# Performance work log

Measured on AMD Instinct MI355X. Metric: run time of the kernel, lower is better.

The kernel has to match this reference:

```python
import jax, jax.numpy as jnp
import numpy as np

VOCAB = 32000
NUM_STATE = 256
NLABEL = 64
BATCH = 128
MAXLEN = 256
# transition init scale chosen so E[e^2]*S*a^2/3 ~= 1 -> per-step magnitude ~constant
TRANS_A = 0.208


def setup_inputs() -> dict:
    key = jax.random.key(0)
    k1, k2, k3, k4 = jax.random.split(key, 4)
    sentences = jax.random.randint(k1, (BATCH, MAXLEN), 0, VOCAB, dtype=jnp.int64)
    # original init: input.weight ~ U(0.5, 0.5) (constant 0.5). Use U(0.25, 0.75) so the
    # emission stays bounded away from 0 (it is divided by) while not being degenerate.
    emb = jax.random.uniform(k2, (VOCAB, NUM_STATE), minval=0.25, maxval=0.75, dtype=jnp.float32)
    transition = jax.random.uniform(k3, (NUM_STATE, NUM_STATE), minval=-TRANS_A, maxval=TRANS_A, dtype=jnp.float32)
    output = jax.random.uniform(k4, (NUM_STATE, NLABEL), minval=-0.5, maxval=0.5, dtype=jnp.float32)
    return {"sentences": sentences, "emb": emb, "transition": transition, "output": output}


def reference(sentences, emb, transition, output):
    # emission: [maxlen, batch, num_state]
    em = emb[sentences.T]

    def step_fwd(carry, e):  # carry: [B,S]
        nxt = jnp.einsum('ij,bj->bi', transition, carry) * e
        return nxt, nxt

    _, fw_rest = jax.lax.scan(step_fwd, em[0], em[1:])
    forwards = jnp.concatenate([em[:1], fw_rest], axis=0)  # [L,B,S]

    em_rev = em[::-1]

    def step_bwd(carry, e):  # uses transition^T
        nxt = jnp.einsum('ji,bj->bi', transition, carry) * e
        return nxt, nxt

    _, bw_rest = jax.lax.scan(step_bwd, em_rev[0], em_rev[1:])
    backwards = jnp.concatenate([em_rev[:1], bw_rest], axis=0)[::-1]  # time-aligned [L,B,S]

    expected_count = forwards * backwards / em
    score = jnp.einsum('lbs,sn->lbn', expected_count, output)
    return score.transpose(1, 0, 2)  # [batch, maxlen, nlabel]
```

## Files before the change

### kernel.cpp

```cpp
#include <hip/hip_runtime.h>
#include <hip/hip_bf16.h>


typedef _Float16 half8 __attribute__((ext_vector_type(8)));
typedef _Float16 half4 __attribute__((ext_vector_type(4)));
typedef __bf16 bf16x8 __attribute__((ext_vector_type(8)));
typedef __bf16 bf16x4 __attribute__((ext_vector_type(4)));
typedef float  f32x4  __attribute__((ext_vector_type(4)));
typedef unsigned long long u64;

#define LL 256
#define BB 128
#define SS 256
#define BT 16
#define RSTR8 67
#define LO_SCALE 2048.0f
#define LO_UNSCALE 4.8828125e-4f

static __device__ __forceinline__ f32x4 mfma16f(half8 a, half8 b, f32x4 c) {
  return __builtin_amdgcn_mfma_f32_16x16x32_f16(a, b, c, 0, 0, 0);
}
static __device__ __forceinline__ f32x4 mfma16(bf16x8 a, bf16x8 b, f32x4 c) {
  return __builtin_amdgcn_mfma_f32_16x16x32_bf16(a, b, c, 0, 0, 0);
}

static __device__ __forceinline__ void lds_barrier() {
  __asm__ __volatile__("s_waitcnt lgkmcnt(0)\n\ts_barrier" ::: "memory");
}

static __device__ __forceinline__ half8 read_frag_h(const u64* plane, int m, int kt, int q) {
  const int o = m * RSTR8 + kt * 8 + q * 2;
  union { u64 u[2]; half8 v; } x;
  x.u[0] = plane[o];
  x.u[1] = plane[o + 1];
  return x.v;
}
static __device__ __forceinline__ bf16x8 read_frag_b(const u64* plane, int m, int kt, int q) {
  const int o = m * RSTR8 + kt * 8 + q * 2;
  union { u64 u[2]; bf16x8 v; } x;
  x.u[0] = plane[o];
  x.u[1] = plane[o + 1];
  return x.v;
}

static __device__ __forceinline__ void write_h4f(u64* plane, int m, int c8, half4 h) {
  union { half4 v; u64 u; } x;
  x.v = h;
  plane[m * RSTR8 + c8] = x.u;
}
static __device__ __forceinline__ void write_h4b(u64* plane, int m, int c8, bf16x4 h) {
  union { bf16x4 v; u64 u; } x;
  x.v = h;
  plane[m * RSTR8 + c8] = x.u;
}

__global__ __launch_bounds__(512, 2)
void hmm_chain(const int* __restrict__ sent, const float* __restrict__ emb,
               const float* __restrict__ T, float* __restrict__ fwbuf,
               float* __restrict__ gbuf)
{
  __shared__ u64 s_carry[2][BT * RSTR8];
  __shared__ int s_tok[BT * 257];

  const int tid  = threadIdx.x;
  const int lane = tid & 63;
  const int w    = tid >> 6;
  const int m    = lane & 15;
  const int q    = lane >> 4;

  const int  bid = blockIdx.x;
  const bool fwd = (bid < 8);
  const int  bg0 = (fwd ? bid : bid - 8) * BT;
  float* const obuf = fwd ? fwbuf : gbuf;

  for (int idx = tid; idx < BT * LL; idx += 512) {
    int bb = idx >> 8, l2 = idx & 255;
    s_tok[bb * 257 + l2] = sent[(bg0 + bb) * LL + l2];
  }
  __syncthreads();

  half8 a_hi[2][8], a_lo[2][8];
#pragma unroll
  for (int mt = 0; mt < 2; ++mt) {
#pragma unroll
    for (int kt = 0; kt < 8; ++kt) {
      const int r0 = 32 * w + 16 * mt + m;
      const int kb = 32 * kt + 8 * q;
      float v[8];
      if (fwd) {
        f32x4 f0 = *(const f32x4*)(T + r0 * 256 + kb);
        f32x4 f1 = *(const f32x4*)(T + r0 * 256 + kb + 4);
#pragma unroll
        for (int j = 0; j < 4; ++j) { v[j] = f0[j]; v[4 + j] = f1[j]; }
      } else {
#pragma unroll
        for (int j = 0; j < 8; ++j) v[j] = T[(kb + j) * 256 + r0];
      }
      half8 hi, lo;
#pragma unroll
      for (int j = 0; j < 8; ++j) {
        _Float16 h = (_Float16)v[j];
        hi[j] = h;
        lo[j] = (_Float16)((v[j] - (float)h) * LO_SCALE);
      }
      a_hi[mt][kt] = hi; a_lo[mt][kt] = lo;
    }
  }

  const int l0 = fwd ? 0 : (LL - 1);
  {
    const int tok0 = s_tok[m * 257 + l0];
#pragma unroll
    for (int mt = 0; mt < 2; ++mt) {
      const int st = 32 * w + 16 * mt + 4 * q;
      f32x4 e0 = *(const f32x4*)(emb + (size_t)tok0 * 256 + st);
      f32x4 outv = e0;
      if (!fwd) outv = 1.0f;
      *(f32x4*)(obuf + ((size_t)(l0 * BB + bg0 + m)) * 256 + st) = outv;
      half4 h4;
#pragma unroll
      for (int r = 0; r < 4; ++r) h4[r] = (_Float16)e0[r];
      const int c8 = 8 * w + 4 * mt + q;
      write_h4f(&s_carry[0][0], m, c8, h4);
    }
  }

  f32x4 em_pref[2];
  {
    const int l1 = fwd ? 1 : (LL - 2);
    const int tok1 = s_tok[m * 257 + l1];
#pragma unroll
    for (int mt = 0; mt < 2; ++mt)
      em_pref[mt] = *(const f32x4*)(emb + (size_t)tok1 * 256 + 32 * w + 16 * mt + 4 * q);
  }
  __syncthreads();

  for (int s = 1; s < LL; ++s) {
    const int l  = fwd ? s : (LL - 1) - s;
    const int rb = (s - 1) & 1, wb = s & 1;

    const u64* pr = &s_carry[rb][0];

    half8 bfr[8];
#pragma unroll
    for (int kt = 0; kt < 8; ++kt)
      bfr[kt] = read_frag_h(pr, m, kt, q);

    f32x4 hh0 = 0.0f, lh0 = 0.0f;
    f32x4 hh1 = 0.0f, lh1 = 0.0f;
#pragma unroll
    for (int kt = 0; kt < 8; ++kt) {
      hh0 = mfma16f(a_hi[0][kt], bfr[kt], hh0);
      hh1 = mfma16f(a_hi[1][kt], bfr[kt], hh1);
      lh0 = mfma16f(a_lo[0][kt], bfr[kt], lh0);
      lh1 = mfma16f(a_lo[1][kt], bfr[kt], lh1);
    }
    f32x4 acc[2];
    acc[0] = hh0 + lh0 * LO_UNSCALE;
    acc[1] = hh1 + lh1 * LO_UNSCALE;

    f32x4 em_now[2];
#pragma unroll
    for (int mt = 0; mt < 2; ++mt) em_now[mt] = em_pref[mt];
    {
      const int ln = fwd ? (s + 1 < LL ? s + 1 : LL - 1)
                         : ((LL - 2) - s > 0 ? (LL - 2) - s : 0);
      const int tokn = s_tok[m * 257 + ln];
#pragma unroll
      for (int mt = 0; mt < 2; ++mt)
        em_pref[mt] = *(const f32x4*)(emb + (size_t)tokn * 256 + 32 * w + 16 * mt + 4 * q);
    }

    u64* pw = &s_carry[wb][0];
    f32x4 sv[2];
#pragma unroll
    for (int mt = 0; mt < 2; ++mt) {
      f32x4 v  = acc[mt];
      f32x4 cn = v * em_now[mt];
      sv[mt]   = fwd ? cn : v;
      half4 h4;
#pragma unroll
      for (int r = 0; r < 4; ++r) h4[r] = (_Float16)cn[r];
      const int c8 = 8 * w + 4 * mt + q;
      write_h4f(pw, m, c8, h4);
    }
#pragma unroll
    for (int mt = 0; mt < 2; ++mt) {
      const int st = 32 * w + 16 * mt + 4 * q;
      *(f32x4*)(obuf + ((size_t)(l * BB + bg0 + m)) * 256 + st) = sv[mt];
    }
    lds_barrier();
  }
}

__global__ __launch_bounds__(256, 2)
void hmm_score(const float* __restrict__ fwbuf, const float* __restrict__ gbuf,
               const float* __restrict__ outm, float* __restrict__ score)
{
  __shared__ u64 p_hi[64 * RSTR8];
  __shared__ u64 p_lo[64 * RSTR8];

  const int tid  = threadIdx.x;
  const int lane = tid & 63;
  const int w    = tid >> 6;
  const int rh   = w >> 1;
  const int np   = w & 1;
  const int m    = lane & 15;
  const int q    = lane >> 4;
  const int R0   = blockIdx.x * 64;

  bf16x8 o_hi[8][2], o_lo[8][2];
#pragma unroll
  for (int kt = 0; kt < 8; ++kt) {
#pragma unroll
    for (int jn = 0; jn < 2; ++jn) {
      bf16x8 hi, lo;
#pragma unroll
      for (int j = 0; j < 8; ++j) {
        float vv = outm[(32 * kt + 8 * q + j) * 64 + 16 * (2 * np + jn) + m];
        __bf16 h = (__bf16)vv;
        hi[j] = h;
        lo[j] = (__bf16)(vv - (float)h);
      }
      o_hi[kt][jn] = hi; o_lo[kt][jn] = lo;
    }
  }

  for (int idx = tid; idx < 64 * 64; idx += 256) {
    int row = idx >> 6, c = idx & 63;
    f32x4 f  = *(const f32x4*)(fwbuf + ((size_t)(R0 + row)) * 256 + c * 4);
    f32x4 gg = *(const f32x4*)(gbuf  + ((size_t)(R0 + row)) * 256 + c * 4);
    f32x4 p = f * gg;
    bf16x4 h4, l4;
#pragma unroll
    for (int r = 0; r < 4; ++r) {
      __bf16 h = (__bf16)p[r];
      h4[r] = h;
      l4[r] = (__bf16)(p[r] - (float)h);
    }
    write_h4b(p_hi, row, c, h4);
    write_h4b(p_lo, row, c, l4);
  }
  lds_barrier();

  f32x4 acc[2][2];
#pragma unroll
  for (int j = 0; j < 2; ++j)
#pragma unroll
    for (int jn = 0; jn < 2; ++jn) acc[j][jn] = 0.0f;

#pragma unroll
  for (int kt = 0; kt < 8; ++kt) {
#pragma unroll
    for (int j = 0; j < 2; ++j) {
      const int row = 32 * rh + 16 * j + m;
      bf16x8 ph = read_frag_b(p_hi, row, kt, q);
      bf16x8 pl = read_frag_b(p_lo, row, kt, q);
#pragma unroll
      for (int jn = 0; jn < 2; ++jn) {
        acc[j][jn] = mfma16(ph, o_hi[kt][jn], acc[j][jn]);
        acc[j][jn] = mfma16(ph, o_lo[kt][jn], acc[j][jn]);
        acc[j][jn] = mfma16(pl, o_hi[kt][jn], acc[j][jn]);
      }
    }
  }

#pragma unroll
  for (int j = 0; j < 2; ++j) {
#pragma unroll
    for (int jn = 0; jn < 2; ++jn) {
#pragma unroll
      for (int r = 0; r < 4; ++r) {
        int row = R0 + 32 * rh + 16 * j + 4 * q + r;
        int l = row >> 7, b = row & 127;
        score[(size_t)b * 16384 + l * 64 + 16 * (2 * np + jn) + m] = acc[j][jn][r];
      }
    }
  }
}

extern "C" void kernel_launch(void* const* d_in, const int* in_sizes, int n_in,
                              void* d_out, int out_size, void* d_ws, size_t ws_size,
                              hipStream_t stream) {
  (void)in_sizes; (void)n_in; (void)out_size; (void)ws_size;
  const int*   sent = (const int*)d_in[0];
  const float* emb  = (const float*)d_in[1];
  const float* T    = (const float*)d_in[2];
  const float* outm = (const float*)d_in[3];
  float* fw = (float*)d_ws;
  float* g  = fw + (size_t)LL * BB * SS;

  hmm_chain<<<16, 512, 0, stream>>>(sent, emb, T, fw, g);
  hmm_score<<<512, 256, 0, stream>>>(fw, g, outm, (float*)d_out);
}
```

Baseline: 325.1 us.

## Store chain intermediates in fp16, unroll chain loop, simplify score GEMM

The forward and backward chain outputs are now written as fp16 instead of fp32, which halves intermediate traffic. The score kernel multiplies the two fp16 operands directly and runs a 2-MFMA hi/lo fp16 split instead of a 3-MFMA bf16 split. The chain loop is unrolled by two with ping-pong registers, and tokens come straight from global memory rather than through an LDS staging step. Output stores are also deferred by one step to overlap with the MFMA work. The risk is precision loss from fp16 storage of forward and backward values and from the fp16 product, including possible overflow or underflow.

```diff
diff --git a/kernel.cpp b/kernel.cpp
--- a/kernel.cpp
+++ b/kernel.cpp
@@ -4,9 +4,7 @@
 
 typedef _Float16 half8 __attribute__((ext_vector_type(8)));
 typedef _Float16 half4 __attribute__((ext_vector_type(4)));
-typedef __bf16 bf16x8 __attribute__((ext_vector_type(8)));
-typedef __bf16 bf16x4 __attribute__((ext_vector_type(4)));
-typedef float  f32x4  __attribute__((ext_vector_type(4)));
+typedef float    f32x4 __attribute__((ext_vector_type(4)));
 typedef unsigned long long u64;
 
 #define LL 256
@@ -20,12 +18,18 @@
 static __device__ __forceinline__ f32x4 mfma16f(half8 a, half8 b, f32x4 c) {
   return __builtin_amdgcn_mfma_f32_16x16x32_f16(a, b, c, 0, 0, 0);
 }
-static __device__ __forceinline__ f32x4 mfma16(bf16x8 a, bf16x8 b, f32x4 c) {
-  return __builtin_amdgcn_mfma_f32_16x16x32_bf16(a, b, c, 0, 0, 0);
-}
 
 static __device__ __forceinline__ void lds_barrier() {
   __asm__ __volatile__("s_waitcnt lgkmcnt(0)\n\ts_barrier" ::: "memory");
+}
+
+static __device__ __forceinline__ u64 pack4(f32x4 v) {
+  union { half4 h; u64 u; } x;
+  x.h[0] = (_Float16)v[0];
+  x.h[1] = (_Float16)v[1];
+  x.h[2] = (_Float16)v[2];
+  x.h[3] = (_Float16)v[3];
+  return x.u;
 }
 
 static __device__ __forceinline__ half8 read_frag_h(const u64* plane, int m, int kt, int q) {
@@ -35,32 +39,49 @@
   x.u[1] = plane[o + 1];
   return x.v;
 }
-static __device__ __forceinline__ bf16x8 read_frag_b(const u64* plane, int m, int kt, int q) {
-  const int o = m * RSTR8 + kt * 8 + q * 2;
-  union { u64 u[2]; bf16x8 v; } x;
-  x.u[0] = plane[o];
-  x.u[1] = plane[o + 1];
-  return x.v;
-}
-
-static __device__ __forceinline__ void write_h4f(u64* plane, int m, int c8, half4 h) {
-  union { half4 v; u64 u; } x;
-  x.v = h;
-  plane[m * RSTR8 + c8] = x.u;
-}
-static __device__ __forceinline__ void write_h4b(u64* plane, int m, int c8, bf16x4 h) {
-  union { bf16x4 v; u64 u; } x;
-  x.v = h;
-  plane[m * RSTR8 + c8] = x.u;
-}
+
+#define CHAIN_STEP(RB, EMC, EMN, TOKC, TOKN, SVC, SVN, DO_STORE)               \
+  {                                                                            \
+    const u64* cb = &s_carry[RB][0];                                           \
+    half8 bfr[8];                                                              \
+    _Pragma("unroll")                                                          \
+    for (int kt = 0; kt < 8; ++kt) bfr[kt] = read_frag_h(cb, m, kt, q);        \
+    if (DO_STORE) {                                                            \
+      *(u64*)(optr)      = SVC[0];                                             \
+      *(u64*)(optr + 16) = SVC[1];                                             \
+      optr += dl;                                                              \
+    }                                                                          \
+    EMN[0] = *(const f32x4*)(emb + (size_t)TOKC * 256 + 32 * w + 4 * q);       \
+    EMN[1] = *(const f32x4*)(emb + (size_t)TOKC * 256 + 32 * w + 16 + 4 * q);  \
+    TOKN = sent_row[tl];                                                       \
+    tl = fwd ? (tl < LL - 1 ? tl + 1 : LL - 1) : (tl > 0 ? tl - 1 : 0);        \
+    f32x4 hh0 = 0.0f, lh0 = 0.0f, hh1 = 0.0f, lh1 = 0.0f;                      \
+    _Pragma("unroll")                                                          \
+    for (int kt = 0; kt < 8; ++kt) {                                           \
+      hh0 = mfma16f(a_hi[0][kt], bfr[kt], hh0);                                \
+      hh1 = mfma16f(a_hi[1][kt], bfr[kt], hh1);                                \
+      lh0 = mfma16f(a_lo[0][kt], bfr[kt], lh0);                                \
+      lh1 = mfma16f(a_lo[1][kt], bfr[kt], lh1);                                \
+    }                                                                          \
+    f32x4 v0 = hh0 + lh0 * LO_UNSCALE;                                         \
+    f32x4 v1 = hh1 + lh1 * LO_UNSCALE;                                         \
+    f32x4 c0 = v0 * EMC[0];                                                    \
+    f32x4 c1 = v1 * EMC[1];                                                    \
+    u64 p0 = pack4(c0), p1 = pack4(c1);                                        \
+    u64* wbuf = &s_carry[RB ^ 1][0];                                           \
+    wbuf[m * RSTR8 + 8 * w + q]     = p0;                                      \
+    wbuf[m * RSTR8 + 8 * w + 4 + q] = p1;                                      \
+    SVN[0] = fwd ? p0 : pack4(v0);                                             \
+    SVN[1] = fwd ? p1 : pack4(v1);                                             \
+    lds_barrier();                                                             \
+  }
 
 __global__ __launch_bounds__(512, 2)
 void hmm_chain(const int* __restrict__ sent, const float* __restrict__ emb,
-               const float* __restrict__ T, float* __restrict__ fwbuf,
-               float* __restrict__ gbuf)
+               const float* __restrict__ T, _Float16* __restrict__ fwh,
+               _Float16* __restrict__ gh)
 {
   __shared__ u64 s_carry[2][BT * RSTR8];
-  __shared__ int s_tok[BT * 257];
 
   const int tid  = threadIdx.x;
   const int lane = tid & 63;
@@ -71,13 +92,8 @@
   const int  bid = blockIdx.x;
   const bool fwd = (bid < 8);
   const int  bg0 = (fwd ? bid : bid - 8) * BT;
-  float* const obuf = fwd ? fwbuf : gbuf;
-
-  for (int idx = tid; idx < BT * LL; idx += 512) {
-    int bb = idx >> 8, l2 = idx & 255;
-    s_tok[bb * 257 + l2] = sent[(bg0 + bb) * LL + l2];
-  }
-  __syncthreads();
+  _Float16* const obuf = fwd ? fwh : gh;
+  const int* const sent_row = sent + (size_t)(bg0 + m) * LL;
 
   half8 a_hi[2][8], a_lo[2][8];
 #pragma unroll
@@ -109,96 +125,48 @@
 
   const int l0 = fwd ? 0 : (LL - 1);
   {
-    const int tok0 = s_tok[m * 257 + l0];
+    const int tok0 = sent_row[l0];
 #pragma unroll
     for (int mt = 0; mt < 2; ++mt) {
       const int st = 32 * w + 16 * mt + 4 * q;
       f32x4 e0 = *(const f32x4*)(emb + (size_t)tok0 * 256 + st);
-      f32x4 outv = e0;
-      if (!fwd) outv = 1.0f;
-      *(f32x4*)(obuf + ((size_t)(l0 * BB + bg0 + m)) * 256 + st) = outv;
-      half4 h4;
-#pragma unroll
-      for (int r = 0; r < 4; ++r) h4[r] = (_Float16)e0[r];
-      const int c8 = 8 * w + 4 * mt + q;
-      write_h4f(&s_carry[0][0], m, c8, h4);
-    }
-  }
-
-  f32x4 em_pref[2];
+      u64 pc = pack4(e0);
+      f32x4 one = 1.0f;
+      u64 po = fwd ? pc : pack4(one);
+      *(u64*)(obuf + (size_t)(l0 * BB + bg0 + m) * SS + st) = po;
+      s_carry[0][m * RSTR8 + 8 * w + 4 * mt + q] = pc;
+    }
+  }
+
+  const int l1 = fwd ? 1 : (LL - 2);
+  f32x4 em_a[2], em_b[2];
   {
-    const int l1 = fwd ? 1 : (LL - 2);
-    const int tok1 = s_tok[m * 257 + l1];
-#pragma unroll
-    for (int mt = 0; mt < 2; ++mt)
-      em_pref[mt] = *(const f32x4*)(emb + (size_t)tok1 * 256 + 32 * w + 16 * mt + 4 * q);
-  }
+    const int tok1 = sent_row[l1];
+    em_a[0] = *(const f32x4*)(emb + (size_t)tok1 * 256 + 32 * w + 4 * q);
+    em_a[1] = *(const f32x4*)(emb + (size_t)tok1 * 256 + 32 * w + 16 + 4 * q);
+  }
+  int tok_a = sent_row[fwd ? 2 : LL - 3];
+  int tok_b;
+  int tl = fwd ? 3 : LL - 4;
+  const int dl = fwd ? BB * SS : -(BB * SS);
+  _Float16* optr = obuf + (size_t)(l1 * BB + bg0 + m) * SS + 32 * w + 4 * q;
+  u64 sv_a[2], sv_b[2];
   __syncthreads();
 
-  for (int s = 1; s < LL; ++s) {
-    const int l  = fwd ? s : (LL - 1) - s;
-    const int rb = (s - 1) & 1, wb = s & 1;
-
-    const u64* pr = &s_carry[rb][0];
-
-    half8 bfr[8];
-#pragma unroll
-    for (int kt = 0; kt < 8; ++kt)
-      bfr[kt] = read_frag_h(pr, m, kt, q);
-
-    f32x4 hh0 = 0.0f, lh0 = 0.0f;
-    f32x4 hh1 = 0.0f, lh1 = 0.0f;
-#pragma unroll
-    for (int kt = 0; kt < 8; ++kt) {
-      hh0 = mfma16f(a_hi[0][kt], bfr[kt], hh0);
-      hh1 = mfma16f(a_hi[1][kt], bfr[kt], hh1);
-      lh0 = mfma16f(a_lo[0][kt], bfr[kt], lh0);
-      lh1 = mfma16f(a_lo[1][kt], bfr[kt], lh1);
-    }
-    f32x4 acc[2];
-    acc[0] = hh0 + lh0 * LO_UNSCALE;
-    acc[1] = hh1 + lh1 * LO_UNSCALE;
-
-    f32x4 em_now[2];
-#pragma unroll
-    for (int mt = 0; mt < 2; ++mt) em_now[mt] = em_pref[mt];
-    {
-      const int ln = fwd ? (s + 1 < LL ? s + 1 : LL - 1)
-                         : ((LL - 2) - s > 0 ? (LL - 2) - s : 0);
-      const int tokn = s_tok[m * 257 + ln];
-#pragma unroll
-      for (int mt = 0; mt < 2; ++mt)
-        em_pref[mt] = *(const f32x4*)(emb + (size_t)tokn * 256 + 32 * w + 16 * mt + 4 * q);
-    }
-
-    u64* pw = &s_carry[wb][0];
-    f32x4 sv[2];
-#pragma unroll
-    for (int mt = 0; mt < 2; ++mt) {
-      f32x4 v  = acc[mt];
-      f32x4 cn = v * em_now[mt];
-      sv[mt]   = fwd ? cn : v;
-      half4 h4;
-#pragma unroll
-      for (int r = 0; r < 4; ++r) h4[r] = (_Float16)cn[r];
-      const int c8 = 8 * w + 4 * mt + q;
-      write_h4f(pw, m, c8, h4);
-    }
-#pragma unroll
-    for (int mt = 0; mt < 2; ++mt) {
-      const int st = 32 * w + 16 * mt + 4 * q;
-      *(f32x4*)(obuf + ((size_t)(l * BB + bg0 + m)) * 256 + st) = sv[mt];
-    }
-    lds_barrier();
-  }
+  CHAIN_STEP(0, em_a, em_b, tok_a, tok_b, sv_b, sv_a, 0)
+  for (int sp = 0; sp < 127; ++sp) {
+    CHAIN_STEP(1, em_b, em_a, tok_b, tok_a, sv_a, sv_b, 1)
+    CHAIN_STEP(0, em_a, em_b, tok_a, tok_b, sv_b, sv_a, 1)
+  }
+  *(u64*)(optr)      = sv_a[0];
+  *(u64*)(optr + 16) = sv_a[1];
 }
 
 __global__ __launch_bounds__(256, 2)
-void hmm_score(const float* __restrict__ fwbuf, const float* __restrict__ gbuf,
+void hmm_score(const _Float16* __restrict__ fwh, const _Float16* __restrict__ gh,
                const float* __restrict__ outm, float* __restrict__ score)
 {
-  __shared__ u64 p_hi[64 * RSTR8];
-  __shared__ u64 p_lo[64 * RSTR8];
+  __shared__ u64 p_pl[64 * RSTR8];
 
   const int tid  = threadIdx.x;
   const int lane = tid & 63;
@@ -209,18 +177,18 @@
   const int q    = lane >> 4;
   const int R0   = blockIdx.x * 64;
 
-  bf16x8 o_hi[8][2], o_lo[8][2];
+  half8 o_hi[8][2], o_lo[8][2];
 #pragma unroll
   for (int kt = 0; kt < 8; ++kt) {
 #pragma unroll
     for (int jn = 0; jn < 2; ++jn) {
-      bf16x8 hi, lo;
+      half8 hi, lo;
 #pragma unroll
       for (int j = 0; j < 8; ++j) {
         float vv = outm[(32 * kt + 8 * q + j) * 64 + 16 * (2 * np + jn) + m];
-        __bf16 h = (__bf16)vv;
+        _Float16 h = (_Float16)vv;
         hi[j] = h;
-        lo[j] = (__bf16)(vv - (float)h);
+        lo[j] = (_Float16)((vv - (float)h) * LO_SCALE);
       }
       o_hi[kt][jn] = hi; o_lo[kt][jn] = lo;
     }
@@ -228,39 +196,30 @@
 
   for (int idx = tid; idx < 64 * 64; idx += 256) {
     int row = idx >> 6, c = idx & 63;
-    f32x4 f  = *(const f32x4*)(fwbuf + ((size_t)(R0 + row)) * 256 + c * 4);
-    f32x4 gg = *(const f32x4*)(gbuf  + ((size_t)(R0 + row)) * 256 + c * 4);
-    f32x4 p = f * gg;
-    bf16x4 h4, l4;
-#pragma unroll
-    for (int r = 0; r < 4; ++r) {
-      __bf16 h = (__bf16)p[r];
-      h4[r] = h;
-      l4[r] = (__bf16)(p[r] - (float)h);
-    }
-    write_h4b(p_hi, row, c, h4);
-    write_h4b(p_lo, row, c, l4);
+    union { u64 u; half4 h; } a, b, p;
+    a.u = *(const u64*)(fwh + (size_t)(R0 + row) * 256 + c * 4);
+    b.u = *(const u64*)(gh  + (size_t)(R0 + row) * 256 + c * 4);
+    p.h = a.h * b.h;
+    p_pl[row * RSTR8 + c] = p.u;
   }
   lds_barrier();
 
-  f32x4 acc[2][2];
+  f32x4 hh[2][2], lh[2][2];
 #pragma unroll
   for (int j = 0; j < 2; ++j)
 #pragma unroll
-    for (int jn = 0; jn < 2; ++jn) acc[j][jn] = 0.0f;
+    for (int jn = 0; jn < 2; ++jn) { hh[j][jn] = 0.0f; lh[j][jn] = 0.0f; }
 
 #pragma unroll
   for (int kt = 0; kt < 8; ++kt) {
 #pragma unroll
     for (int j = 0; j < 2; ++j) {
       const int row = 32 * rh + 16 * j + m;
-      bf16x8 ph = read_frag_b(p_hi, row, kt, q);
-      bf16x8 pl = read_frag_b(p_lo, row, kt, q);
+      half8 pf = read_frag_h(p_pl, row, kt, q);
 #pragma unroll
       for (int jn = 0; jn < 2; ++jn) {
-        acc[j][jn] = mfma16(ph, o_hi[kt][jn], acc[j][jn]);
-        acc[j][jn] = mfma16(ph, o_lo[kt][jn], acc[j][jn]);
-        acc[j][jn] = mfma16(pl, o_hi[kt][jn], acc[j][jn]);
+        hh[j][jn] = mfma16f(pf, o_hi[kt][jn], hh[j][jn]);
+        lh[j][jn] = mfma16f(pf, o_lo[kt][jn], lh[j][jn]);
       }
     }
   }
@@ -269,11 +228,12 @@
   for (int j = 0; j < 2; ++j) {
 #pragma unroll
     for (int jn = 0; jn < 2; ++jn) {
+      f32x4 acc = hh[j][jn] + lh[j][jn] * LO_UNSCALE;
 #pragma unroll
       for (int r = 0; r < 4; ++r) {
         int row = R0 + 32 * rh + 16 * j + 4 * q + r;
         int l = row >> 7, b = row & 127;
-        score[(size_t)b * 16384 + l * 64 + 16 * (2 * np + jn) + m] = acc[j][jn][r];
+        score[(size_t)b * 16384 + l * 64 + 16 * (2 * np + jn) + m] = acc[r];
       }
     }
   }
@@ -287,9 +247,9 @@
   const float* emb  = (const float*)d_in[1];
   const float* T    = (const float*)d_in[2];
   const float* outm = (const float*)d_in[3];
-  float* fw = (float*)d_ws;
-  float* g  = fw + (size_t)LL * BB * SS;
-
-  hmm_chain<<<16, 512, 0, stream>>>(sent, emb, T, fw, g);
-  hmm_score<<<512, 256, 0, stream>>>(fw, g, outm, (float*)d_out);
-}
+  _Float16* fwh = (_Float16*)d_ws;
+  _Float16* gh  = fwh + (size_t)LL * BB * SS;
+
+  hmm_chain<<<16, 512, 0, stream>>>(sent, emb, T, fwh, gh);
+  hmm_score<<<512, 256, 0, stream>>>(fwh, gh, outm, (float*)d_out);
+}
```

New measurement: 339.8 us. 1.05x slower.
